# Performance work log

Hardware: AMD Instinct MI355X
Metric: run time of the kernel (lower is better)

## Reference

```python
import jax, jax.numpy as jnp
import numpy as np

N_NODES = 100000
N_EDGES = 3200000
F_IN, F_HID, F_OUT = 1433, 8, 7
K = 2  # kernel_size, dim=1, degree-1 B-spline -> basis (1-u, u)
LEAKY_SLOPE = 0.2


def att_spline_conv(x, edge_index, pseudo, w, root, att, bias, n_nodes):
    """Attention SplineConv layer (dim=1, kernel_size=2, linear B-spline).

    w:    [K, in, out] spline kernel weights
    root: [in, out]    root/self weight
    att:  [2*out]      attention vector (src-message part || dst part)
    """
    src, dst = edge_index[0], edge_index[1]
    u = pseudo[:, 0]                                   # [E], in [0,1]
    basis = jnp.stack([1.0 - u, u], axis=1)            # [E, K]
    # transform at node level first (cheap), then gather per edge
    xw = jnp.einsum('ni,kio->nko', x, w)               # [N, K, out]
    m = jnp.einsum('ek,eko->eo', basis, xw[src])       # [E, out] spline message
    h = x @ root                                       # [N, out] root transform
    out_dim = w.shape[-1]
    # GAT-style attention: leaky_relu(a_src . m_e + a_dst . h_dst)
    score = m @ att[:out_dim] + (h @ att[out_dim:])[dst]   # [E]
    score = jax.nn.leaky_relu(score, LEAKY_SLOPE)
    smax = jax.ops.segment_max(score, dst, num_segments=n_nodes)
    e = jnp.exp(score - smax[dst])
    denom = jax.ops.segment_sum(e, dst, num_segments=n_nodes)
    alpha = e / (denom[dst] + 1e-16)                   # segment softmax over dst
    agg = jax.ops.segment_sum(alpha[:, None] * m, dst, num_segments=n_nodes)
    return agg + h + bias


def setup_inputs() -> dict:
    key = jax.random.key(0)
    ks = jax.random.split(key, 12)
    x = jax.random.normal(ks[0], (N_NODES, F_IN), dtype=jnp.float32)
    edge_index = jax.random.randint(ks[1], (2, N_EDGES), 0, N_NODES, dtype=jnp.int64)
    pseudo = jax.random.uniform(ks[2], (N_EDGES, 1), dtype=jnp.float32)
    s1 = 1.0 / np.sqrt(F_IN)
    s2 = 1.0 / np.sqrt(F_HID)
    return {
        'x': x,
        'edge_index': edge_index,
        'pseudo': pseudo,
        'w1': jax.random.normal(ks[3], (K, F_IN, F_HID), dtype=jnp.float32) * s1,
        'root1': jax.random.normal(ks[4], (F_IN, F_HID), dtype=jnp.float32) * s1,
        'att1': jax.random.normal(ks[5], (2 * F_HID,), dtype=jnp.float32) * s2,
        'bias1': jnp.zeros((F_HID,), dtype=jnp.float32),
        'w2': jax.random.normal(ks[6], (K, F_HID, F_OUT), dtype=jnp.float32) * s2,
        'root2': jax.random.normal(ks[7], (F_HID, F_OUT), dtype=jnp.float32) * s2,
        'att2': jax.random.normal(ks[8], (2 * F_OUT,), dtype=jnp.float32) * s2,
        'bias2': jnp.zeros((F_OUT,), dtype=jnp.float32),
    }


def reference(x, edge_index, pseudo, w1, root1, att1, bias1, w2, root2, att2, bias2):
    # eval mode: F.dropout with training=False is identity
    n = x.shape[0]
    h = jax.nn.elu(att_spline_conv(x, edge_index, pseudo, w1, root1, att1, bias1, n))
    h = att_spline_conv(h, edge_index, pseudo, w2, root2, att2, bias2, n)
    return jax.nn.log_softmax(h, axis=1)
```

## Files before the change

### kernel.cpp

```cpp
#include <hip/hip_runtime.h>
#include <math.h>

#define TPB 256
#define F_IN 1433
#define KPAD 1440
#define NT 45
#define NFULL 44
#define BROWS 64

typedef __attribute__((ext_vector_type(8))) short bf16x8;
typedef __attribute__((ext_vector_type(4))) float f32x4;

static __device__ __forceinline__ short f2bf(float f) {
    unsigned u = __float_as_uint(f);
    unsigned r = (u + 0x7FFFu + ((u >> 16) & 1u)) >> 16;
    return (short)r;
}

__global__ __launch_bounds__(256) void prep_kernel(
    const float* __restrict__ w1, const float* __restrict__ root1,
    short* __restrict__ WT, int* __restrict__ cnt, int N)
{
    int i = blockIdx.x * 256 + threadIdx.x;
    if (i < N) cnt[i] = 0;
    if (i < 32 * KPAD) {
        int col = i / KPAD, k = i - col * KPAD;
        float v = 0.f;
        if (k < F_IN) {
            if (col < 8)       v = w1[(size_t)k * 8 + col];
            else if (col < 16) v = w1[(size_t)(F_IN + k) * 8 + (col - 8)];
            else if (col < 24) v = root1[(size_t)k * 8 + (col - 16)];
        }
        WT[i] = f2bf(v);
    }
}

__global__ __launch_bounds__(256) void node1_hist_kernel(
    const float* __restrict__ x,
    const short* __restrict__ WT,
    const float* __restrict__ att1,
    float* __restrict__ XW1,
    float* __restrict__ H1,
    float2* __restrict__ SC1,
    float* __restrict__ HA1,
    const int* __restrict__ ei,
    int* __restrict__ cnt,
    int N, int E, int NB1)
{
    __shared__ float dump[BROWS * 25];

    const int tid = threadIdx.x;
    const int bid = blockIdx.x;

    if (bid >= NB1) {
        int e = (bid - NB1) * TPB + tid;
        if (e < E) atomicAdd(&cnt[ei[(size_t)E + e]], 1);
        return;
    }

    const int wv   = tid >> 6;
    const int lane = tid & 63;
    const int rowbase = bid * BROWS;

    const int r0 = lane & 15;
    const int kg = lane >> 4;
    const int klane = kg * 8;
    int rr = rowbase + wv * 16 + r0;
    if (rr >= N) rr = N - 1;
    const float* xr = x + (size_t)rr * F_IN;
    const short* wt0 = WT + (size_t)r0 * KPAD + klane;
    const short* wt1 = wt0 + 16 * KPAD;

    f32x4 acc0, acc1;
#pragma unroll
    for (int r = 0; r < 4; ++r) { acc0[r] = 0.f; acc1[r] = 0.f; }

#define LOADT(t, Aa, Ab, Ba, Bb) do {                                          \
        const float* p_ = xr + (t) * 32 + klane;                               \
        Aa = *reinterpret_cast<const float4*>(p_);                             \
        Ab = *reinterpret_cast<const float4*>(p_ + 4);                         \
        Ba = *reinterpret_cast<const bf16x8*>(wt0 + (t) * 32);                 \
        Bb = *reinterpret_cast<const bf16x8*>(wt1 + (t) * 32);                 \
    } while (0)

#define COMP(Aa, Ab, Ba, Bb) do {                                              \
        bf16x8 pa_;                                                            \
        pa_[0] = f2bf(Aa.x); pa_[1] = f2bf(Aa.y);                              \
        pa_[2] = f2bf(Aa.z); pa_[3] = f2bf(Aa.w);                              \
        pa_[4] = f2bf(Ab.x); pa_[5] = f2bf(Ab.y);                              \
        pa_[6] = f2bf(Ab.z); pa_[7] = f2bf(Ab.w);                              \
        acc0 = __builtin_amdgcn_mfma_f32_16x16x32_bf16(pa_, Ba, acc0, 0, 0, 0);\
        acc1 = __builtin_amdgcn_mfma_f32_16x16x32_bf16(pa_, Bb, acc1, 0, 0, 0);\
    } while (0)

    float4 A00, A01, A10, A11, A20, A21, A30, A31;
    bf16x8 B00, B01, B10, B11, B20, B21, B30, B31;

    LOADT(0, A00, A01, B00, B01);
    LOADT(1, A10, A11, B10, B11);
    LOADT(2, A20, A21, B20, B21);
    LOADT(3, A30, A31, B30, B31);

    for (int t = 0; t < NFULL; t += 4) {
        COMP(A00, A01, B00, B01);
        if (t + 4 < NFULL) LOADT(t + 4, A00, A01, B00, B01);
        COMP(A10, A11, B10, B11);
        if (t + 5 < NFULL) LOADT(t + 5, A10, A11, B10, B11);
        COMP(A20, A21, B20, B21);
        if (t + 6 < NFULL) LOADT(t + 6, A20, A21, B20, B21);
        COMP(A30, A31, B30, B31);
        if (t + 7 < NFULL) LOADT(t + 7, A30, A31, B30, B31);
    }
#undef LOADT
#undef COMP

    {
        const int kf = NFULL * 32 + klane;
        bf16x8 pa;
#pragma unroll
        for (int q = 0; q < 8; ++q) {
            float v = (kf + q < F_IN) ? xr[kf + q] : 0.f;
            pa[q] = f2bf(v);
        }
        bf16x8 b0 = *reinterpret_cast<const bf16x8*>(wt0 + NFULL * 32);
        bf16x8 b1 = *reinterpret_cast<const bf16x8*>(wt1 + NFULL * 32);
        acc0 = __builtin_amdgcn_mfma_f32_16x16x32_bf16(pa, b0, acc0, 0, 0, 0);
        acc1 = __builtin_amdgcn_mfma_f32_16x16x32_bf16(pa, b1, acc1, 0, 0, 0);
    }

#pragma unroll
    for (int ot = 0; ot < 2; ++ot) {
        int col = ot * 16 + (lane & 15);
        if (col < 24) {
#pragma unroll
            for (int r = 0; r < 4; ++r) {
                int row = wv * 16 + kg * 4 + r;
                dump[row * 25 + col] = (ot == 0) ? acc0[r] : acc1[r];
            }
        }
    }
    __syncthreads();

    if (tid < BROWS) {
        int n = rowbase + tid;
        if (n < N) {
            float sum[24];
#pragma unroll
            for (int j = 0; j < 24; ++j) sum[j] = dump[tid * 25 + j];
            float s0 = 0.f, s1 = 0.f, ha = 0.f;
#pragma unroll
            for (int j = 0; j < 8; ++j) {
                s0 += sum[j] * att1[j];
                s1 += sum[8 + j] * att1[j];
                ha += sum[16 + j] * att1[8 + j];
            }
            float4* xwout = reinterpret_cast<float4*>(XW1 + (size_t)n * 16);
            xwout[0] = make_float4(sum[0], sum[1], sum[2], sum[3]);
            xwout[1] = make_float4(sum[4], sum[5], sum[6], sum[7]);
            xwout[2] = make_float4(sum[8], sum[9], sum[10], sum[11]);
            xwout[3] = make_float4(sum[12], sum[13], sum[14], sum[15]);
            float4* hout = reinterpret_cast<float4*>(H1 + (size_t)n * 8);
            hout[0] = make_float4(sum[16], sum[17], sum[18], sum[19]);
            hout[1] = make_float4(sum[20], sum[21], sum[22], sum[23]);
            SC1[n] = make_float2(s0, s1);
            HA1[n] = ha;
        }
    }
}

__global__ __launch_bounds__(256) void scanA_kernel(
    const int* __restrict__ cnt, int* __restrict__ rowptr, int* __restrict__ bsums, int N)
{
    __shared__ int lds[256];
    int t = threadIdx.x;
    int base = blockIdx.x * 1024 + t * 4;
    int c[4];
#pragma unroll
    for (int j = 0; j < 4; ++j) c[j] = (base + j < N) ? cnt[base + j] : 0;
    int tsum = c[0] + c[1] + c[2] + c[3];
    lds[t] = tsum;
    __syncthreads();
    for (int off = 1; off < 256; off <<= 1) {
        int v = (t >= off) ? lds[t - off] : 0;
        __syncthreads();
        lds[t] += v;
        __syncthreads();
    }
    int run = lds[t] - tsum;
#pragma unroll
    for (int j = 0; j < 4; ++j) {
        if (base + j < N) rowptr[base + j] = run;
        run += c[j];
    }
    if (t == 255) bsums[blockIdx.x] = lds[255];
}

__global__ __launch_bounds__(128) void scanB_kernel(int* __restrict__ bsums, int nb)
{
    __shared__ int lds[128];
    int t = threadIdx.x;
    int v = (t < nb) ? bsums[t] : 0;
    lds[t] = v;
    __syncthreads();
    for (int off = 1; off < 128; off <<= 1) {
        int w = (t >= off) ? lds[t - off] : 0;
        __syncthreads();
        lds[t] += w;
        __syncthreads();
    }
    if (t < nb) bsums[t] = lds[t] - v;
}

__global__ __launch_bounds__(256) void scanC_kernel(
    int* __restrict__ rowptr, int* __restrict__ cnt, const int* __restrict__ bsums, int N, int E)
{
    int i = blockIdx.x * TPB + threadIdx.x;
    if (i < N) {
        int v = rowptr[i] + bsums[i >> 10];
        rowptr[i] = v;
        cnt[i] = v;
    }
    if (i == 0) rowptr[N] = E;
}

__global__ __launch_bounds__(256) void scatter_kernel(
    const int* __restrict__ ei, const float* __restrict__ pseudo,
    int* __restrict__ cursor, int2* __restrict__ recs, int E)
{
    int e = blockIdx.x * TPB + threadIdx.x;
    if (e >= E) return;
    int s = ei[e];
    int d = ei[(size_t)E + e];
    float u = pseudo[e];
    int pos = atomicAdd(&cursor[d], 1);
    recs[pos] = make_int2(s, __float_as_int(u));
}

__global__ __launch_bounds__(256) void gather1_kernel(
    const int* __restrict__ rowptr, const int2* __restrict__ recs,
    const float4* __restrict__ XW1v,
    const float2* __restrict__ SC1, const float* __restrict__ HA1,
    const float* __restrict__ H1, const float* __restrict__ bias1,
    const float* __restrict__ w2, const float* __restrict__ root2, const float* __restrict__ att2,
    float* __restrict__ XW2, float* __restrict__ H2, float2* __restrict__ SC2, float* __restrict__ HA2,
    int N)
{
    int tid = blockIdx.x * TPB + threadIdx.x;
    int n = tid >> 4;
    int lane = tid & 15;
    if (n >= N) return;
    int start = rowptr[n], end = rowptr[n + 1];
    float ha = HA1[n];
    float den = 0.f;
    float num[8];
#pragma unroll
    for (int j = 0; j < 8; ++j) num[j] = 0.f;

    for (int i = start + lane; i < end; i += 16) {
        int2 r = recs[i];
        int s = r.x;
        float u = __int_as_float(r.y);
        float um = 1.f - u;
        float2 sc = SC1[s];
        float raw = um * sc.x + u * sc.y + ha;
        float score = (raw > 0.f) ? raw : 0.2f * raw;
        float w = __expf(score);
        const float4* xw = XW1v + (size_t)s * 4;
        float4 p0 = xw[0], p1 = xw[1], q0 = xw[2], q1 = xw[3];
        num[0] = fmaf(w, um * p0.x + u * q0.x, num[0]);
        num[1] = fmaf(w, um * p0.y + u * q0.y, num[1]);
        num[2] = fmaf(w, um * p0.z + u * q0.z, num[2]);
        num[3] = fmaf(w, um * p0.w + u * q0.w, num[3]);
        num[4] = fmaf(w, um * p1.x + u * q1.x, num[4]);
        num[5] = fmaf(w, um * p1.y + u * q1.y, num[5]);
        num[6] = fmaf(w, um * p1.z + u * q1.z, num[6]);
        num[7] = fmaf(w, um * p1.w + u * q1.w, num[7]);
        den += w;
    }
#pragma unroll
    for (int off = 1; off < 16; off <<= 1) {
#pragma unroll
        for (int j = 0; j < 8; ++j) num[j] += __shfl_xor(num[j], off);
        den += __shfl_xor(den, off);
    }
    if (lane != 0) return;

    float inv = 1.f / (den + 1e-16f);
    float hp[8];
#pragma unroll
    for (int j = 0; j < 8; ++j) {
        float o = num[j] * inv + H1[(size_t)n * 8 + j] + bias1[j];
        hp[j] = (o > 0.f) ? o : expm1f(o);
    }
    float a[7], b[7], h[7];
#pragma unroll
    for (int j2 = 0; j2 < 7; ++j2) { a[j2] = 0.f; b[j2] = 0.f; h[j2] = 0.f; }
#pragma unroll
    for (int j = 0; j < 8; ++j) {
#pragma unroll
        for (int j2 = 0; j2 < 7; ++j2) {
            a[j2] = fmaf(hp[j], w2[j * 7 + j2], a[j2]);
            b[j2] = fmaf(hp[j], w2[56 + j * 7 + j2], b[j2]);
            h[j2] = fmaf(hp[j], root2[j * 7 + j2], h[j2]);
        }
    }
    float s0 = 0.f, s1 = 0.f, hA = 0.f;
#pragma unroll
    for (int j2 = 0; j2 < 7; ++j2) {
        s0 += a[j2] * att2[j2];
        s1 += b[j2] * att2[j2];
        hA += h[j2] * att2[7 + j2];
    }
    float4* xwout = reinterpret_cast<float4*>(XW2 + (size_t)n * 16);
    xwout[0] = make_float4(a[0], a[1], a[2], a[3]);
    xwout[1] = make_float4(a[4], a[5], a[6], 0.f);
    xwout[2] = make_float4(b[0], b[1], b[2], b[3]);
    xwout[3] = make_float4(b[4], b[5], b[6], 0.f);
    float4* hout = reinterpret_cast<float4*>(H2 + (size_t)n * 8);
    hout[0] = make_float4(h[0], h[1], h[2], h[3]);
    hout[1] = make_float4(h[4], h[5], h[6], 0.f);
    SC2[n] = make_float2(s0, s1);
    HA2[n] = hA;
}

__global__ __launch_bounds__(256) void gather2_kernel(
    const int* __restrict__ rowptr, const int2* __restrict__ recs,
    const float4* __restrict__ XW2v,
    const float2* __restrict__ SC2, const float* __restrict__ HA2,
    const float* __restrict__ H2, const float* __restrict__ bias2,
    float* __restrict__ out, int N)
{
    int tid = blockIdx.x * TPB + threadIdx.x;
    int n = tid >> 4;
    int lane = tid & 15;
    if (n >= N) return;
    int start = rowptr[n], end = rowptr[n + 1];
    float ha = HA2[n];
    float den = 0.f;
    float num[7];
#pragma unroll
    for (int j = 0; j < 7; ++j) num[j] = 0.f;

    for (int i = start + lane; i < end; i += 16) {
        int2 r = recs[i];
        int s = r.x;
        float u = __int_as_float(r.y);
        float um = 1.f - u;
        float2 sc = SC2[s];
        float raw = um * sc.x + u * sc.y + ha;
        float score = (raw > 0.f) ? raw : 0.2f * raw;
        float w = __expf(score);
        const float4* xw = XW2v + (size_t)s * 4;
        float4 p0 = xw[0], p1 = xw[1], q0 = xw[2], q1 = xw[3];
        num[0] = fmaf(w, um * p0.x + u * q0.x, num[0]);
        num[1] = fmaf(w, um * p0.y + u * q0.y, num[1]);
        num[2] = fmaf(w, um * p0.z + u * q0.z, num[2]);
        num[3] = fmaf(w, um * p0.w + u * q0.w, num[3]);
        num[4] = fmaf(w, um * p1.x + u * q1.x, num[4]);
        num[5] = fmaf(w, um * p1.y + u * q1.y, num[5]);
        num[6] = fmaf(w, um * p1.z + u * q1.z, num[6]);
        den += w;
    }
#pragma unroll
    for (int off = 1; off < 16; off <<= 1) {
#pragma unroll
        for (int j = 0; j < 7; ++j) num[j] += __shfl_xor(num[j], off);
        den += __shfl_xor(den, off);
    }
    if (lane != 0) return;

    float inv = 1.f / (den + 1e-16f);
    float o[7];
    float mx = -1e30f;
#pragma unroll
    for (int j = 0; j < 7; ++j) {
        o[j] = fmaf(num[j], inv, H2[(size_t)n * 8 + j] + bias2[j]);
        mx = fmaxf(mx, o[j]);
    }
    float sum = 0.f;
#pragma unroll
    for (int j = 0; j < 7; ++j) sum += __expf(o[j] - mx);
    float lse = mx + __logf(sum);
#pragma unroll
    for (int j = 0; j < 7; ++j) out[(size_t)n * 7 + j] = o[j] - lse;
}

extern "C" void kernel_launch(void* const* d_in, const int* in_sizes, int n_in,
                              void* d_out, int out_size, void* d_ws, size_t ws_size,
                              hipStream_t stream) {
    const float* x      = (const float*)d_in[0];
    const int*   ei     = (const int*)d_in[1];
    const float* pseudo = (const float*)d_in[2];
    const float* w1     = (const float*)d_in[3];
    const float* root1  = (const float*)d_in[4];
    const float* att1   = (const float*)d_in[5];
    const float* bias1  = (const float*)d_in[6];
    const float* w2     = (const float*)d_in[7];
    const float* root2  = (const float*)d_in[8];
    const float* att2   = (const float*)d_in[9];
    const float* bias2  = (const float*)d_in[10];

    const int N = in_sizes[0] / F_IN;
    const int E = in_sizes[2];
    const size_t Ns = (size_t)N;

    float* ws   = (float*)d_ws;
    float* XW1  = ws;
    float* H1   = XW1 + 16 * Ns;
    float2* SC1 = (float2*)(H1 + 8 * Ns);
    float* HA1  = (float*)SC1 + 2 * Ns;
    float* XW2  = HA1 + Ns;
    float* H2   = XW2 + 16 * Ns;
    float2* SC2 = (float2*)(H2 + 8 * Ns);
    float* HA2  = (float*)SC2 + 2 * Ns;
    int*   cnt    = (int*)(HA2 + Ns);
    int*   rowptr = cnt + Ns;
    int*   bsums  = rowptr + Ns + 1;
    size_t off = (size_t)(bsums + 128) - (size_t)d_ws;
    off = (off + 7) & ~(size_t)7;
    int2*  recs = (int2*)((char*)d_ws + off);
    size_t woff = off + (size_t)E * sizeof(int2);
    woff = (woff + 15) & ~(size_t)15;
    short* WT = (short*)((char*)d_ws + woff);

    int nblk  = (N + TPB - 1) / TPB;
    int eblk  = (E + TPB - 1) / TPB;
    int sblkA = (N + 1023) / 1024;
    int nb1   = (N + BROWS - 1) / BROWS;
    int gblk  = ((N * 16) + TPB - 1) / TPB;
    int prepn = (32 * KPAD > N) ? 32 * KPAD : N;
    int pblk  = (prepn + TPB - 1) / TPB;

    prep_kernel<<<pblk, TPB, 0, stream>>>(w1, root1, WT, cnt, N);
    node1_hist_kernel<<<nb1 + eblk, TPB, 0, stream>>>(
        x, WT, att1, XW1, H1, SC1, HA1, ei, cnt, N, E, nb1);
    scanA_kernel<<<sblkA, TPB, 0, stream>>>(cnt, rowptr, bsums, N);
    scanB_kernel<<<1, 128, 0, stream>>>(bsums, sblkA);
    scanC_kernel<<<nblk, TPB, 0, stream>>>(rowptr, cnt, bsums, N, E);
    scatter_kernel<<<eblk, TPB, 0, stream>>>(ei, pseudo, cnt, recs, E);
    gather1_kernel<<<gblk, TPB, 0, stream>>>(rowptr, recs, (const float4*)XW1, SC1, HA1,
                                             H1, bias1, w2, root2, att2,
                                             XW2, H2, SC2, HA2, N);
    gather2_kernel<<<gblk, TPB, 0, stream>>>(rowptr, recs, (const float4*)XW2, SC2, HA2,
                                             H2, bias2, (float*)d_out, N);
}
```

Measured before the change: 645.9 us.

## Stage x rows into LDS via async global_load_lds with double buffering

Replaces direct per-lane register loads of x rows in the first-layer node GEMM with asynchronous global-to-LDS copies, organised into 128-wide K chunks with double buffering and an XOR swizzle. Weight fragments are prefetched one chunk ahead, and manual waitcnts are used for the pipeline. The intent is more coalesced, deeper in-flight loads of the 570MB x matrix to approach memory bandwidth. The cost is 64KB of LDS per block, which lowers occupancy, and fragile hand-written waitcnt ordering.

```diff
diff --git a/kernel.cpp b/kernel.cpp
--- a/kernel.cpp
+++ b/kernel.cpp
@@ -4,8 +4,8 @@
 #define TPB 256
 #define F_IN 1433
 #define KPAD 1440
-#define NT 45
-#define NFULL 44
+#define NCH 11
+#define TK 1408
 #define BROWS 64
 
 typedef __attribute__((ext_vector_type(8))) short bf16x8;
@@ -15,6 +15,13 @@
     unsigned u = __float_as_uint(f);
     unsigned r = (u + 0x7FFFu + ((u >> 16) & 1u)) >> 16;
     return (short)r;
+}
+
+static __device__ __forceinline__ void gl2lds16(const float* g, float* l) {
+    __builtin_amdgcn_global_load_lds(
+        (const __attribute__((address_space(1))) void*)g,
+        (__attribute__((address_space(3))) void*)l,
+        16, 0, 0);
 }
 
 __global__ __launch_bounds__(256) void prep_kernel(
@@ -47,7 +54,7 @@
     int* __restrict__ cnt,
     int N, int E, int NB1)
 {
-    __shared__ float dump[BROWS * 25];
+    __shared__ float xb[4][2][2048];
 
     const int tid = threadIdx.x;
     const int bid = blockIdx.x;
@@ -60,77 +67,116 @@
 
     const int wv   = tid >> 6;
     const int lane = tid & 63;
-    const int rowbase = bid * BROWS;
+    const int rowbase = bid * BROWS + wv * 16;
+
+    const int half = lane >> 5;
+    const int u    = lane & 31;
+    const int su   = u >> 3;
+    const int mu   = (u >> 1) & 3;
+    const int lowb = (u & 1) * 4;
+    const float* dsrc[8];
+#pragma unroll
+    for (int i = 0; i < 8; ++i) {
+        int rl = i * 2 + half;
+        int r = rowbase + rl; if (r >= N) r = N - 1;
+        int goff = su * 32 + ((mu ^ (rl & 3)) * 8) + lowb;
+        dsrc[i] = x + (size_t)r * F_IN + goff;
+    }
+
+#define ISSUE(c, buf) do {                                                      \
+        float* lb_ = &xb[wv][buf][0];                                           \
+        _Pragma("unroll")                                                       \
+        for (int i = 0; i < 8; ++i)                                             \
+            gl2lds16(dsrc[i] + (c) * 128, lb_ + i * 256);                       \
+    } while (0)
 
     const int r0 = lane & 15;
     const int kg = lane >> 4;
-    const int klane = kg * 8;
-    int rr = rowbase + wv * 16 + r0;
-    if (rr >= N) rr = N - 1;
-    const float* xr = x + (size_t)rr * F_IN;
-    const short* wt0 = WT + (size_t)r0 * KPAD + klane;
+    const int aoff = r0 * 128 + ((kg ^ (r0 & 3)) * 8);
+    const short* wt0 = WT + (size_t)r0 * KPAD + kg * 8;
     const short* wt1 = wt0 + 16 * KPAD;
 
+#define WTLOAD(c, W) do {                                                       \
+        _Pragma("unroll")                                                       \
+        for (int s = 0; s < 4; ++s) {                                           \
+            W[s][0] = *reinterpret_cast<const bf16x8*>(wt0 + (c) * 128 + s * 32); \
+            W[s][1] = *reinterpret_cast<const bf16x8*>(wt1 + (c) * 128 + s * 32); \
+        }                                                                       \
+    } while (0)
+
     f32x4 acc0, acc1;
 #pragma unroll
     for (int r = 0; r < 4; ++r) { acc0[r] = 0.f; acc1[r] = 0.f; }
 
-#define LOADT(t, Aa, Ab, Ba, Bb) do {                                          \
-        const float* p_ = xr + (t) * 32 + klane;                               \
-        Aa = *reinterpret_cast<const float4*>(p_);                             \
-        Ab = *reinterpret_cast<const float4*>(p_ + 4);                         \
-        Ba = *reinterpret_cast<const bf16x8*>(wt0 + (t) * 32);                 \
-        Bb = *reinterpret_cast<const bf16x8*>(wt1 + (t) * 32);                 \
+    bf16x8 WA[4][2], WB[4][2];
+
+    ISSUE(0, 0);
+    __builtin_amdgcn_sched_barrier(0);
+    ISSUE(1, 1);
+    __builtin_amdgcn_sched_barrier(0);
+    WTLOAD(0, WA);
+
+#define CHUNK(c, buf, Wcur, Wnxt) do {                                          \
+        asm volatile("s_waitcnt vmcnt(16)" ::: "memory");                       \
+        const float* Bb_ = &xb[wv][buf][0];                                     \
+        float4 fa0 = *reinterpret_cast<const float4*>(Bb_ + aoff + 0 * 32);     \
+        float4 fb0 = *reinterpret_cast<const float4*>(Bb_ + aoff + 0 * 32 + 4); \
+        float4 fa1 = *reinterpret_cast<const float4*>(Bb_ + aoff + 1 * 32);     \
+        float4 fb1 = *reinterpret_cast<const float4*>(Bb_ + aoff + 1 * 32 + 4); \
+        float4 fa2 = *reinterpret_cast<const float4*>(Bb_ + aoff + 2 * 32);     \
+        float4 fb2 = *reinterpret_cast<const float4*>(Bb_ + aoff + 2 * 32 + 4); \
+        float4 fa3 = *reinterpret_cast<const float4*>(Bb_ + aoff + 3 * 32);     \
+        float4 fb3 = *reinterpret_cast<const float4*>(Bb_ + aoff + 3 * 32 + 4); \
+        asm volatile("s_waitcnt lgkmcnt(0)" ::: "memory");                      \
+        if ((c) + 2 < NCH) { ISSUE((c) + 2, buf); }                             \
+        if ((c) + 1 < NCH) { WTLOAD((c) + 1, Wnxt); }                           \
+        bf16x8 pa;                                                              \
+        pa[0]=f2bf(fa0.x); pa[1]=f2bf(fa0.y); pa[2]=f2bf(fa0.z); pa[3]=f2bf(fa0.w); \
+        pa[4]=f2bf(fb0.x); pa[5]=f2bf(fb0.y); pa[6]=f2bf(fb0.z); pa[7]=f2bf(fb0.w); \
+        acc0 = __builtin_amdgcn_mfma_f32_16x16x32_bf16(pa, Wcur[0][0], acc0, 0, 0, 0); \
+        acc1 = __builtin_amdgcn_mfma_f32_16x16x32_bf16(pa, Wcur[0][1], acc1, 0, 0, 0); \
+        pa[0]=f2bf(fa1.x); pa[1]=f2bf(fa1.y); pa[2]=f2bf(fa1.z); pa[3]=f2bf(fa1.w); \
+        pa[4]=f2bf(fb1.x); pa[5]=f2bf(fb1.y); pa[6]=f2bf(fb1.z); pa[7]=f2bf(fb1.w); \
+        acc0 = __builtin_amdgcn_mfma_f32_16x16x32_bf16(pa, Wcur[1][0], acc0, 0, 0, 0); \
+        acc1 = __builtin_amdgcn_mfma_f32_16x16x32_bf16(pa, Wcur[1][1], acc1, 0, 0, 0); \
+        pa[0]=f2bf(fa2.x); pa[1]=f2bf(fa2.y); pa[2]=f2bf(fa2.z); pa[3]=f2bf(fa2.w); \
+        pa[4]=f2bf(fb2.x); pa[5]=f2bf(fb2.y); pa[6]=f2bf(fb2.z); pa[7]=f2bf(fb2.w); \
+        acc0 = __builtin_amdgcn_mfma_f32_16x16x32_bf16(pa, Wcur[2][0], acc0, 0, 0, 0); \
+        acc1 = __builtin_amdgcn_mfma_f32_16x16x32_bf16(pa, Wcur[2][1], acc1, 0, 0, 0); \
+        pa[0]=f2bf(fa3.x); pa[1]=f2bf(fa3.y); pa[2]=f2bf(fa3.z); pa[3]=f2bf(fa3.w); \
+        pa[4]=f2bf(fb3.x); pa[5]=f2bf(fb3.y); pa[6]=f2bf(fb3.z); pa[7]=f2bf(fb3.w); \
+        acc0 = __builtin_amdgcn_mfma_f32_16x16x32_bf16(pa, Wcur[3][0], acc0, 0, 0, 0); \
+        acc1 = __builtin_amdgcn_mfma_f32_16x16x32_bf16(pa, Wcur[3][1], acc1, 0, 0, 0); \
     } while (0)
 
-#define COMP(Aa, Ab, Ba, Bb) do {                                              \
-        bf16x8 pa_;                                                            \
-        pa_[0] = f2bf(Aa.x); pa_[1] = f2bf(Aa.y);                              \
-        pa_[2] = f2bf(Aa.z); pa_[3] = f2bf(Aa.w);                              \
-        pa_[4] = f2bf(Ab.x); pa_[5] = f2bf(Ab.y);                              \
-        pa_[6] = f2bf(Ab.z); pa_[7] = f2bf(Ab.w);                              \
-        acc0 = __builtin_amdgcn_mfma_f32_16x16x32_bf16(pa_, Ba, acc0, 0, 0, 0);\
-        acc1 = __builtin_amdgcn_mfma_f32_16x16x32_bf16(pa_, Bb, acc1, 0, 0, 0);\
-    } while (0)
-
-    float4 A00, A01, A10, A11, A20, A21, A30, A31;
-    bf16x8 B00, B01, B10, B11, B20, B21, B30, B31;
-
-    LOADT(0, A00, A01, B00, B01);
-    LOADT(1, A10, A11, B10, B11);
-    LOADT(2, A20, A21, B20, B21);
-    LOADT(3, A30, A31, B30, B31);
-
-    for (int t = 0; t < NFULL; t += 4) {
-        COMP(A00, A01, B00, B01);
-        if (t + 4 < NFULL) LOADT(t + 4, A00, A01, B00, B01);
-        COMP(A10, A11, B10, B11);
-        if (t + 5 < NFULL) LOADT(t + 5, A10, A11, B10, B11);
-        COMP(A20, A21, B20, B21);
-        if (t + 6 < NFULL) LOADT(t + 6, A20, A21, B20, B21);
-        COMP(A30, A31, B30, B31);
-        if (t + 7 < NFULL) LOADT(t + 7, A30, A31, B30, B31);
-    }
-#undef LOADT
-#undef COMP
+    for (int c = 0; c < NCH; c += 2) {
+        CHUNK(c, 0, WA, WB);
+        if (c + 1 < NCH) CHUNK(c + 1, 1, WB, WA);
+    }
+#undef CHUNK
+#undef WTLOAD
+#undef ISSUE
 
     {
-        const int kf = NFULL * 32 + klane;
+        int rr = rowbase + r0; if (rr >= N) rr = N - 1;
+        const float* xr = x + (size_t)rr * F_IN;
+        const int kf = TK + kg * 8;
         bf16x8 pa;
 #pragma unroll
-        for (int q = 0; q < 8; ++q) {
-            float v = (kf + q < F_IN) ? xr[kf + q] : 0.f;
-            pa[q] = f2bf(v);
-        }
-        bf16x8 b0 = *reinterpret_cast<const bf16x8*>(wt0 + NFULL * 32);
-        bf16x8 b1 = *reinterpret_cast<const bf16x8*>(wt1 + NFULL * 32);
+        for (int q = 0; q < 8; ++q)
+            pa[q] = f2bf((kf + q < F_IN) ? xr[kf + q] : 0.f);
+        bf16x8 b0 = *reinterpret_cast<const bf16x8*>(wt0 + TK);
+        bf16x8 b1 = *reinterpret_cast<const bf16x8*>(wt1 + TK);
         acc0 = __builtin_amdgcn_mfma_f32_16x16x32_bf16(pa, b0, acc0, 0, 0, 0);
         acc1 = __builtin_amdgcn_mfma_f32_16x16x32_bf16(pa, b1, acc1, 0, 0, 0);
     }
 
+    __syncthreads();
+
+    float* dump = reinterpret_cast<float*>(xb);
 #pragma unroll
     for (int ot = 0; ot < 2; ++ot) {
-        int col = ot * 16 + (lane & 15);
+        int col = ot * 16 + r0;
         if (col < 24) {
 #pragma unroll
             for (int r = 0; r < 4; ++r) {
@@ -142,7 +188,7 @@
     __syncthreads();
 
     if (tid < BROWS) {
-        int n = rowbase + tid;
+        int n = bid * BROWS + tid;
         if (n < N) {
             float sum[24];
 #pragma unroll
```

Result: faster. 631.5 us (-2.2%).

## Stage x rows through LDS with coalesced loads and double-buffered MFMA phases

Applied to the files above, without the earlier changes.

Reworks the node-level GEMM in node1_hist_kernel. Each wave now loads two full x rows at a time with coalesced float4 loads, converts them to bf16 in a double-buffered LDS staging area, and runs the MFMA over 8 phases, prefetching the next rows while computing. Previously each lane read strided 32-float pieces of 16 different rows. The epilogue now uses wave shuffles instead of an LDS dump plus a single-thread reduction. This uses only 2 of the 16 MFMA rows, so matrix work per row rises, and the LDS footprint grows to about 46KB per block, which can lower occupancy.

```diff
diff --git a/kernel.cpp b/kernel.cpp
--- a/kernel.cpp
+++ b/kernel.cpp
@@ -4,11 +4,12 @@
 #define TPB 256
 #define F_IN 1433
 #define KPAD 1440
-#define NT 45
-#define NFULL 44
+#define NCHUNK 45
 #define BROWS 64
+#define NPH 8
 
 typedef __attribute__((ext_vector_type(8))) short bf16x8;
+typedef __attribute__((ext_vector_type(4))) short s16x4;
 typedef __attribute__((ext_vector_type(4))) float f32x4;
 
 static __device__ __forceinline__ short f2bf(float f) {
@@ -47,7 +48,7 @@
     int* __restrict__ cnt,
     int N, int E, int NB1)
 {
-    __shared__ float dump[BROWS * 25];
+    __shared__ short sb[4][2][2][KPAD];
 
     const int tid = threadIdx.x;
     const int bid = blockIdx.x;
@@ -62,110 +63,101 @@
     const int lane = tid & 63;
     const int rowbase = bid * BROWS;
 
-    const int r0 = lane & 15;
     const int kg = lane >> 4;
-    const int klane = kg * 8;
-    int rr = rowbase + wv * 16 + r0;
-    if (rr >= N) rr = N - 1;
-    const float* xr = x + (size_t)rr * F_IN;
-    const short* wt0 = WT + (size_t)r0 * KPAD + klane;
+    const int rl = ((lane & 15) < 2) ? (lane & 15) : 0;
+    const short* wt0 = WT + (size_t)(lane & 15) * KPAD + kg * 8;
     const short* wt1 = wt0 + 16 * KPAD;
-
-    f32x4 acc0, acc1;
-#pragma unroll
-    for (int r = 0; r < 4; ++r) { acc0[r] = 0.f; acc1[r] = 0.f; }
-
-#define LOADT(t, Aa, Ab, Ba, Bb) do {                                          \
-        const float* p_ = xr + (t) * 32 + klane;                               \
-        Aa = *reinterpret_cast<const float4*>(p_);                             \
-        Ab = *reinterpret_cast<const float4*>(p_ + 4);                         \
-        Ba = *reinterpret_cast<const bf16x8*>(wt0 + (t) * 32);                 \
-        Bb = *reinterpret_cast<const bf16x8*>(wt1 + (t) * 32);                 \
+    const float att1v = att1[lane & 7];
+    const float att1h = att1[8 + (lane & 7)];
+
+    float4 V[2][6];
+    float  vtail[2];
+
+#define STAGE_LOAD(p) do {                                                      \
+        _Pragma("unroll")                                                       \
+        for (int rr = 0; rr < 2; ++rr) {                                        \
+            int grow = rowbase + (p) * 8 + 2 * wv + rr;                         \
+            if (grow >= N) grow = N - 1;                                        \
+            const float* rp = x + (size_t)grow * F_IN;                          \
+            _Pragma("unroll")                                                   \
+            for (int i = 0; i < 6; ++i) {                                       \
+                int ib = (i < 5) ? i * 256 : 1176;                              \
+                V[rr][i] = *reinterpret_cast<const float4*>(rp + ib + lane * 4);\
+            }                                                                   \
+            vtail[rr] = rp[1432];                                               \
+        }                                                                       \
     } while (0)
 
-#define COMP(Aa, Ab, Ba, Bb) do {                                              \
-        bf16x8 pa_;                                                            \
-        pa_[0] = f2bf(Aa.x); pa_[1] = f2bf(Aa.y);                              \
-        pa_[2] = f2bf(Aa.z); pa_[3] = f2bf(Aa.w);                              \
-        pa_[4] = f2bf(Ab.x); pa_[5] = f2bf(Ab.y);                              \
-        pa_[6] = f2bf(Ab.z); pa_[7] = f2bf(Ab.w);                              \
-        acc0 = __builtin_amdgcn_mfma_f32_16x16x32_bf16(pa_, Ba, acc0, 0, 0, 0);\
-        acc1 = __builtin_amdgcn_mfma_f32_16x16x32_bf16(pa_, Bb, acc1, 0, 0, 0);\
+#define CONVERT_WRITE(buf) do {                                                 \
+        _Pragma("unroll")                                                       \
+        for (int rr = 0; rr < 2; ++rr) {                                        \
+            _Pragma("unroll")                                                   \
+            for (int i = 0; i < 6; ++i) {                                       \
+                int kb = ((i < 5) ? i * 256 : 1176) + lane * 4;                 \
+                float4 f = V[rr][i];                                            \
+                s16x4 s;                                                        \
+                s[0] = f2bf(f.x); s[1] = f2bf(f.y);                             \
+                s[2] = f2bf(f.z); s[3] = f2bf(f.w);                             \
+                *reinterpret_cast<s16x4*>(&sb[wv][buf][rr][kb]) = s;            \
+            }                                                                   \
+        }                                                                       \
+        if (lane == 0) {                                                        \
+            _Pragma("unroll")                                                   \
+            for (int rr = 0; rr < 2; ++rr) {                                    \
+                bf16x8 tl;                                                      \
+                tl[0] = f2bf(vtail[rr]);                                        \
+                tl[1] = 0; tl[2] = 0; tl[3] = 0;                                \
+                tl[4] = 0; tl[5] = 0; tl[6] = 0; tl[7] = 0;                     \
+                *reinterpret_cast<bf16x8*>(&sb[wv][buf][rr][1432]) = tl;        \
+            }                                                                   \
+        }                                                                       \
     } while (0)
 
-    float4 A00, A01, A10, A11, A20, A21, A30, A31;
-    bf16x8 B00, B01, B10, B11, B20, B21, B30, B31;
-
-    LOADT(0, A00, A01, B00, B01);
-    LOADT(1, A10, A11, B10, B11);
-    LOADT(2, A20, A21, B20, B21);
-    LOADT(3, A30, A31, B30, B31);
-
-    for (int t = 0; t < NFULL; t += 4) {
-        COMP(A00, A01, B00, B01);
-        if (t + 4 < NFULL) LOADT(t + 4, A00, A01, B00, B01);
-        COMP(A10, A11, B10, B11);
-        if (t + 5 < NFULL) LOADT(t + 5, A10, A11, B10, B11);
-        COMP(A20, A21, B20, B21);
-        if (t + 6 < NFULL) LOADT(t + 6, A20, A21, B20, B21);
-        COMP(A30, A31, B30, B31);
-        if (t + 7 < NFULL) LOADT(t + 7, A30, A31, B30, B31);
-    }
-#undef LOADT
-#undef COMP
-
-    {
-        const int kf = NFULL * 32 + klane;
-        bf16x8 pa;
-#pragma unroll
-        for (int q = 0; q < 8; ++q) {
-            float v = (kf + q < F_IN) ? xr[kf + q] : 0.f;
-            pa[q] = f2bf(v);
+    STAGE_LOAD(0);
+    CONVERT_WRITE(0);
+
+    for (int ph = 0; ph < NPH; ++ph) {
+        if (ph + 1 < NPH) STAGE_LOAD(ph + 1);
+        __builtin_amdgcn_sched_barrier(0);
+
+        const int cb = ph & 1;
+        const short* arow = &sb[wv][cb][rl][0];
+        f32x4 a0, a1;
+#pragma unroll
+        for (int r = 0; r < 4; ++r) { a0[r] = 0.f; a1[r] = 0.f; }
+#pragma unroll
+        for (int t = 0; t < NCHUNK; ++t) {
+            bf16x8 pa = *reinterpret_cast<const bf16x8*>(arow + t * 32 + kg * 8);
+            bf16x8 b0 = *reinterpret_cast<const bf16x8*>(wt0 + t * 32);
+            bf16x8 b1 = *reinterpret_cast<const bf16x8*>(wt1 + t * 32);
+            a0 = __builtin_amdgcn_mfma_f32_16x16x32_bf16(pa, b0, a0, 0, 0, 0);
+            a1 = __builtin_amdgcn_mfma_f32_16x16x32_bf16(pa, b1, a1, 0, 0, 0);
         }
-        bf16x8 b0 = *reinterpret_cast<const bf16x8*>(wt0 + NFULL * 32);
-        bf16x8 b1 = *reinterpret_cast<const bf16x8*>(wt1 + NFULL * 32);
-        acc0 = __builtin_amdgcn_mfma_f32_16x16x32_bf16(pa, b0, acc0, 0, 0, 0);
-        acc1 = __builtin_amdgcn_mfma_f32_16x16x32_bf16(pa, b1, acc1, 0, 0, 0);
-    }
-
-#pragma unroll
-    for (int ot = 0; ot < 2; ++ot) {
-        int col = ot * 16 + (lane & 15);
-        if (col < 24) {
-#pragma unroll
-            for (int r = 0; r < 4; ++r) {
-                int row = wv * 16 + kg * 4 + r;
-                dump[row * 25 + col] = (ot == 0) ? acc0[r] : acc1[r];
+
+        const int n0 = rowbase + ph * 8 + 2 * wv;
+#pragma unroll
+        for (int rr = 0; rr < 2; ++rr) {
+            int n = n0 + rr;
+            if (n < N) {
+                float xw = a0[rr];
+                float hv = a1[rr];
+                float ps = xw * att1v;
+                float pH = hv * att1h;
+                ps += __shfl_xor(ps, 1); pH += __shfl_xor(pH, 1);
+                ps += __shfl_xor(ps, 2); pH += __shfl_xor(pH, 2);
+                ps += __shfl_xor(ps, 4); pH += __shfl_xor(pH, 4);
+                float s1v = __shfl(ps, 8);
+                if (lane < 16) XW1[(size_t)n * 16 + lane] = xw;
+                if (lane < 8)  H1[(size_t)n * 8 + lane] = hv;
+                if (lane == 0) { SC1[n] = make_float2(ps, s1v); HA1[n] = pH; }
             }
         }
-    }
-    __syncthreads();
-
-    if (tid < BROWS) {
-        int n = rowbase + tid;
-        if (n < N) {
-            float sum[24];
-#pragma unroll
-            for (int j = 0; j < 24; ++j) sum[j] = dump[tid * 25 + j];
-            float s0 = 0.f, s1 = 0.f, ha = 0.f;
-#pragma unroll
-            for (int j = 0; j < 8; ++j) {
-                s0 += sum[j] * att1[j];
-                s1 += sum[8 + j] * att1[j];
-                ha += sum[16 + j] * att1[8 + j];
-            }
-            float4* xwout = reinterpret_cast<float4*>(XW1 + (size_t)n * 16);
-            xwout[0] = make_float4(sum[0], sum[1], sum[2], sum[3]);
-            xwout[1] = make_float4(sum[4], sum[5], sum[6], sum[7]);
-            xwout[2] = make_float4(sum[8], sum[9], sum[10], sum[11]);
-            xwout[3] = make_float4(sum[12], sum[13], sum[14], sum[15]);
-            float4* hout = reinterpret_cast<float4*>(H1 + (size_t)n * 8);
-            hout[0] = make_float4(sum[16], sum[17], sum[18], sum[19]);
-            hout[1] = make_float4(sum[20], sum[21], sum[22], sum[23]);
-            SC1[n] = make_float2(s0, s1);
-            HA1[n] = ha;
-        }
-    }
+        __builtin_amdgcn_sched_barrier(0);
+
+        if (ph + 1 < NPH) CONVERT_WRITE((ph + 1) & 1);
+    }
+#undef STAGE_LOAD
+#undef CONVERT_WRITE
 }
 
 __global__ __launch_bounds__(256) void scanA_kernel(
```

Result: slower. 742.0 us (+14.9%).
